# Kernel tuning notes

Hardware: AMD Instinct MI355X
Metric: run time of the kernel (lower is better)

The kernel has to match this reference:

```python
import jax, jax.numpy as jnp
import numpy as np

NUM_ENT, SEQ, H, OUT, NG = 10000, 10, 200, 100, 2048


def _seg_mean(x, idx, n):
    s = jax.ops.segment_sum(x, idx, num_segments=n)
    d = jax.ops.segment_sum(jnp.ones((idx.shape[0],), x.dtype), idx, num_segments=n)
    return s / jnp.maximum(d, 1.0)[:, None]


def setup_inputs() -> dict:
    k = jax.random.split(jax.random.key(0), 24)
    N, E, Nw, Ew, Vw, Rsel, MQ = 50000, 200000, 30000, 300000, 40000, 8192, 8
    f = lambda i, shp: jax.random.normal(k[i], shp, jnp.float32) * 0.05
    ri = lambda i, shp, hi: jax.random.randint(k[i], shp, 0, hi)
    return dict(
        ent_embeds=f(0, (NUM_ENT, H)), rel_embeds=f(1, (240, H)), word_embeds=f(2, (Vw, OUT)),
        gcn_w1=f(3, (OUT, H)), gcn_b1=jnp.zeros((H,), jnp.float32),
        gcn_w2=f(4, (H, H)), gcn_b2=jnp.zeros((H,), jnp.float32),
        cg1_wn=f(5, (H, OUT)), cg1_wl=f(6, (H, OUT)), cg1_wr=f(7, (H, OUT)),
        cg2_wn=f(8, (OUT, H)), cg2_wl=f(9, (OUT, H)), cg2_wr=f(10, (OUT, H)),
        attn_wa=f(11, (H, H)), attn_wc=f(12, (2 * H, H)),
        node_slot=jnp.arange(N), edge_src=ri(13, (E,), N), edge_dst=ri(14, (E,), N),
        edge_type=ri(15, (E,), 240), word_id=ri(16, (Nw,), Vw),
        wsrc=ri(17, (Ew,), Nw), wdst=ri(18, (Ew,), Nw),
        ent_word_idx=ri(19, (N, MQ), Nw), ent_word_mask=ri(20, (N, MQ), 2).astype(jnp.int32),
        rel_word_idx=ri(21, (Rsel, MQ), Nw), rel_word_mask=ri(22, (Rsel, MQ), 2).astype(jnp.int32),
        r_ids_graph=ri(23, (Rsel,), E), edge_slot=jnp.arange(Rsel))


def reference(ent_embeds, rel_embeds, word_embeds, gcn_w1, gcn_b1, gcn_w2, gcn_b2,
              cg1_wn, cg1_wl, cg1_wr, cg2_wn, cg2_wl, cg2_wr, attn_wa, attn_wc,
              node_slot, edge_src, edge_dst, edge_type, word_id, wsrc, wdst,
              ent_word_idx, ent_word_mask, rel_word_idx, rel_word_mask, r_ids_graph, edge_slot):
    N = node_slot.shape[0]
    Nw = word_id.shape[0]
    Rsel = r_ids_graph.shape[0]
    # --- se_aggr: 2-layer GCN over the batched word graph ---
    wh = word_embeds[word_id]                                   # [Nw,100]
    wh = jax.nn.relu(_seg_mean(wh[wsrc], wdst, Nw) @ gcn_w1 + gcn_b1)
    wh = jax.nn.relu(_seg_mean(wh[wsrc], wdst, Nw) @ gcn_w2 + gcn_b2)
    # --- re_aggr1/re_aggr2: CompGCN message passing on batched event graph ---
    h = ent_embeds[node_slot % NUM_ENT]                         # [N,200]
    e = rel_embeds[edge_type]                                   # [E,200]
    def compgcn(h, e, wn, wl, wr):
        agg = _seg_mean(h[edge_src] - e, edge_dst, N)           # sub-composition msgs
        return jax.nn.relu(agg @ wn + h @ wl), e @ wr
    h, e = compgcn(h, e, cg1_wn, cg1_wl, cg1_wr)                # 200 -> 100
    h, e = compgcn(h, e, cg2_wn, cg2_wl, cg2_wr)                # 100 -> 200
    embeds_g_r = e[r_ids_graph]                                 # [Rsel,200]
    # --- build Q_mx / H_mx (padded word-context groups) + 'general' attention ---
    Q = jnp.concatenate([h, embeds_g_r], 0)                     # [N+Rsel,200]
    H_ent = wh[ent_word_idx] * ent_word_mask[..., None].astype(wh.dtype)   # [N,8,200]
    H_rel = wh[rel_word_idx] * rel_word_mask[..., None].astype(wh.dtype)   # [Rsel,8,200]
    Hm = jnp.concatenate([H_ent, H_rel], 0)                     # [N+Rsel,8,200]
    scores = jnp.einsum('md,de,mke->mk', Q, attn_wa, Hm)
    attn = jax.nn.softmax(scores, axis=-1)
    ctx = jnp.einsum('mk,mkd->md', attn, Hm)
    out = jnp.tanh(jnp.concatenate([ctx, Q], -1) @ attn_wc)     # [N+Rsel,200]
    h_out, r_out = out[:N], out[N:]
    # --- temporal scatter of node embeddings per snapshot graph ---
    nid = node_slot % NUM_ENT
    gidx = node_slot // (N // SEQ)
    node_emb_temporal = jnp.zeros((NUM_ENT, SEQ, H), h_out.dtype).at[nid, gidx].set(h_out)
    # --- pack selected edge embeds into padded [NG, SEQ, H] sequence tensor ---
    per = Rsel // NG
    row, pos = edge_slot // per, edge_slot % per
    embed_seq = jnp.zeros((NG, SEQ, H), r_out.dtype).at[row, pos].set(r_out)
    return embed_seq, node_emb_temporal
```

## Files before the change

kernel.cpp:

```cpp
#include <hip/hip_runtime.h>
#include <cstddef>

constexpr int NUM_ENT_C = 10000;
constexpr int SEQ_C     = 10;
constexpr int H_C       = 200;
constexpr int OUT_C     = 100;
constexpr int NG_C      = 2048;
constexpr int NREL_C    = 240;
constexpr int MQ_C      = 8;

typedef __attribute__((ext_vector_type(8))) short          bf16x8;
typedef __attribute__((ext_vector_type(4))) float          f32x4;
typedef __attribute__((ext_vector_type(8))) unsigned short u16x8;

__device__ __forceinline__ unsigned short f2bf(float v) {
    unsigned u = __float_as_uint(v);
    unsigned r = (u + 0x7FFFu + ((u >> 16) & 1u)) >> 16;
    return (unsigned short)r;
}
__device__ __forceinline__ float bf2f(unsigned short b) {
    return __uint_as_float((unsigned)b << 16);
}
__device__ __forceinline__ void up2(unsigned u, float& lo, float& hi) {
    lo = __uint_as_float(u << 16);
    hi = __uint_as_float(u & 0xFFFF0000u);
}

__global__ void prep_k(const float* __restrict__ ent, unsigned short* __restrict__ entb, size_t e8,
                       const float* __restrict__ wemb, unsigned short* __restrict__ wembb, size_t w8,
                       int* __restrict__ cdeg, int nNodes) {
    size_t total = e8 + w8 + (size_t)nNodes;
    size_t stride = (size_t)gridDim.x * blockDim.x;
    for (size_t t = (size_t)blockIdx.x * blockDim.x + threadIdx.x; t < total; t += stride) {
        if (t < e8) {
            const float* s = ent + t * 8;
            u16x8 o;
            #pragma unroll
            for (int i = 0; i < 8; ++i) o[i] = f2bf(s[i]);
            *reinterpret_cast<u16x8*>(entb + t * 8) = o;
        } else if (t < e8 + w8) {
            size_t tt = t - e8;
            const float* s = wemb + tt * 8;
            u16x8 o;
            #pragma unroll
            for (int i = 0; i < 8; ++i) o[i] = f2bf(s[i]);
            *reinterpret_cast<u16x8*>(wembb + tt * 8) = o;
        } else {
            cdeg[t - e8 - w8] = 0;
        }
    }
}

__global__ void hist2_k(const int* __restrict__ wdst, int Ew,
                        const int* __restrict__ edst, int E,
                        int* __restrict__ cdeg, int Nw) {
    int total = Ew + E;
    int stride = gridDim.x * blockDim.x;
    for (int t = blockIdx.x * blockDim.x + threadIdx.x; t < total; t += stride) {
        if (t < Ew) atomicAdd(&cdeg[wdst[t]], 1);
        else        atomicAdd(&cdeg[Nw + edst[t - Ew]], 1);
    }
}

__global__ void scanA_k(const int* __restrict__ v, int* __restrict__ bsum, int n) {
    __shared__ int s[256];
    int t = threadIdx.x;
    int i = blockIdx.x * 256 + t;
    s[t] = (i < n) ? v[i] : 0;
    __syncthreads();
    for (int d = 128; d; d >>= 1) {
        if (t < d) s[t] += s[t + d];
        __syncthreads();
    }
    if (t == 0) bsum[blockIdx.x] = s[0];
}

__global__ void scanB_k(int* __restrict__ bsum, int nb) {
    __shared__ int s[512];
    int t = threadIdx.x;
    int v = (t < nb) ? bsum[t] : 0;
    s[t] = v;
    __syncthreads();
    for (int d = 1; d < 512; d <<= 1) {
        int x = (t >= d) ? s[t - d] : 0;
        __syncthreads();
        s[t] += x;
        __syncthreads();
    }
    if (t < nb) bsum[t] = s[t] - v;
}

__global__ void scanC_k(const int* __restrict__ v, const int* __restrict__ bsum,
                        int* __restrict__ offs, int* __restrict__ cur, int n) {
    __shared__ int s[256];
    int t = threadIdx.x;
    int i = blockIdx.x * 256 + t;
    int val = (i < n) ? v[i] : 0;
    s[t] = val;
    __syncthreads();
    for (int d = 1; d < 256; d <<= 1) {
        int x = (t >= d) ? s[t - d] : 0;
        __syncthreads();
        s[t] += x;
        __syncthreads();
    }
    if (i < n) {
        int ex = s[t] - val + bsum[blockIdx.x];
        offs[i] = ex;
        cur[i]  = ex;
    }
}

__global__ void fill2_k(const int* __restrict__ wdst, const int* __restrict__ wsrc,
                        const int* __restrict__ word_id, int Ew,
                        const int* __restrict__ edst, const int* __restrict__ esrc,
                        const int* __restrict__ etype, int E,
                        int* __restrict__ ccur, int Nw,
                        int* __restrict__ bktA, int* __restrict__ bktB) {
    int total = Ew + E;
    int stride = gridDim.x * blockDim.x;
    for (int t = blockIdx.x * blockDim.x + threadIdx.x; t < total; t += stride) {
        if (t < Ew) {
            int s = wsrc[t];
            int p = atomicAdd(&ccur[wdst[t]], 1);
            bktA[p] = word_id[s];
            bktB[p] = s;
        } else {
            int e = t - Ew;
            int p = atomicAdd(&ccur[Nw + edst[e]], 1);
            bktA[p] = esrc[e];
            bktB[p] = etype[e];
        }
    }
}

template<int K1, int K2, int Kp, bool RELSUB, bool SRCMOD, bool SELFMOD, bool DUAL>
__global__ __launch_bounds__(256) void gather_mean_k(
        const unsigned short* __restrict__ feat, const unsigned short* __restrict__ selfT,
        const float* __restrict__ rel,
        const int* __restrict__ bktS, const int* __restrict__ bktT,
        const int* __restrict__ offs, const int* __restrict__ deg,
        unsigned short* __restrict__ dst, int n) {
    int node = blockIdx.x * 4 + (threadIdx.x >> 6);
    int lane = threadIdx.x & 63;
    if (node >= n) return;
    int off = offs[node], dg = deg[node];
    float acc[4] = {0.f, 0.f, 0.f, 0.f};
    unsigned short* drow = dst + (size_t)node * Kp;

    if (DUAL) {
        int half = lane >> 5, lh = lane & 31;
        int d0 = lh * 4;
        bool act = d0 < K1;
        for (int i = 0; i < dg; i += 2) {
            int ii = i + half;
            if (ii < dg && act) {
                int s = bktS[off + ii];
                if (SRCMOD) s = s % NUM_ENT_C;
                uint2 u = *reinterpret_cast<const uint2*>(feat + (size_t)s * K1 + d0);
                float e0, e1, e2, e3;
                up2(u.x, e0, e1); up2(u.y, e2, e3);
                if (RELSUB) {
                    int tt = bktT[off + ii];
                    float4 rv = *reinterpret_cast<const float4*>(rel + (size_t)tt * K1 + d0);
                    e0 -= rv.x; e1 -= rv.y; e2 -= rv.z; e3 -= rv.w;
                }
                acc[0] += e0; acc[1] += e1; acc[2] += e2; acc[3] += e3;
            }
        }
        #pragma unroll
        for (int c = 0; c < 4; ++c) acc[c] += __shfl_xor(acc[c], 32);
        float inv = 1.f / fmaxf((float)dg, 1.f);
        if (half == 0 && act) {
            uint2 o;
            o.x = (unsigned)f2bf(acc[0] * inv) | ((unsigned)f2bf(acc[1] * inv) << 16);
            o.y = (unsigned)f2bf(acc[2] * inv) | ((unsigned)f2bf(acc[3] * inv) << 16);
            *reinterpret_cast<uint2*>(drow + d0) = o;
        }
        if (K2 > 0 && half == 1 && d0 < K2) {
            int srow = SELFMOD ? (node % NUM_ENT_C) : node;
            uint2 sv = *reinterpret_cast<const uint2*>(selfT + (size_t)srow * K2 + d0);
            *reinterpret_cast<uint2*>(drow + K1 + d0) = sv;
        }
    } else {
        int d0 = lane * 4;
        bool act = d0 < K1;
        for (int i = 0; i < dg; ++i) {
            if (act) {
                int s = bktS[off + i];
                if (SRCMOD) s = s % NUM_ENT_C;
                uint2 u = *reinterpret_cast<const uint2*>(feat + (size_t)s * K1 + d0);
                float e0, e1, e2, e3;
                up2(u.x, e0, e1); up2(u.y, e2, e3);
                if (RELSUB) {
                    int tt = bktT[off + i];
                    float4 rv = *reinterpret_cast<const float4*>(rel + (size_t)tt * K1 + d0);
                    e0 -= rv.x; e1 -= rv.y; e2 -= rv.z; e3 -= rv.w;
                }
                acc[0] += e0; acc[1] += e1; acc[2] += e2; acc[3] += e3;
            }
        }
        float inv = 1.f / fmaxf((float)dg, 1.f);
        if (act) {
            uint2 o;
            o.x = (unsigned)f2bf(acc[0] * inv) | ((unsigned)f2bf(acc[1] * inv) << 16);
            o.y = (unsigned)f2bf(acc[2] * inv) | ((unsigned)f2bf(acc[3] * inv) << 16);
            *reinterpret_cast<uint2*>(drow + d0) = o;
        }
        if (K2 > 0 && d0 < K2) {
            int srow = SELFMOD ? (node % NUM_ENT_C) : node;
            uint2 sv = *reinterpret_cast<const uint2*>(selfT + (size_t)srow * K2 + d0);
            *reinterpret_cast<uint2*>(drow + K1 + d0) = sv;
        }
    }
    for (int cc = K1 + K2 + lane; cc < Kp; cc += 64) drow[cc] = 0;
}

__global__ void convw_all_k(const float* __restrict__ gcn_w1, const float* __restrict__ gcn_w2,
                            const float* __restrict__ cg1_wn, const float* __restrict__ cg1_wl,
                            const float* __restrict__ cg2_wn, const float* __restrict__ cg2_wl,
                            const float* __restrict__ attn_wa, const float* __restrict__ attn_wc,
                            unsigned short* __restrict__ Wt) {
    constexpr int S0 = 26624;
    constexpr int S1 = S0 + 46592;
    constexpr int S2 = S1 + 46592;
    constexpr int S3 = S2 + 46592;
    constexpr int S4 = S3 + 46592;
    constexpr int S5 = S4 + 86528;
    int stride = gridDim.x * blockDim.x;
    for (int t = blockIdx.x * blockDim.x + threadIdx.x; t < S5; t += stride) {
        float v = 0.f;
        if (t < S0) {
            int l = t, nn = l >> 7, k = l & 127;
            if (nn < 200 && k < 100) v = gcn_w1[k * 200 + nn];
        } else if (t < S1) {
            int l = t - S0, nn = l / 224, k = l - nn * 224;
            if (nn < 200 && k < 200) v = gcn_w2[k * 200 + nn];
        } else if (t < S2) {
            int l = t - S1, nn = l / 416, k = l - nn * 416;
            if (nn < 100) {
                if (k < 200)      v = cg1_wn[k * 100 + nn];
                else if (k < 400) v = cg1_wl[(k - 200) * 100 + nn];
            }
        } else if (t < S3) {
            int l = t - S2, nn = l / 224, k = l - nn * 224;
            if (nn < 200) {
                if (k < 100)      v = cg2_wn[k * 200 + nn];
                else if (k < 200) v = cg2_wl[(k - 100) * 200 + nn];
            }
        } else if (t < S4) {
            int l = t - S3, nn = l / 224, k = l - nn * 224;
            if (nn < 200 && k < 200) v = attn_wa[k * 200 + nn];
        } else {
            int l = t - S4, nn = l / 416, k = l - nn * 416;
            if (nn < 200 && k < 400) v = attn_wc[k * 200 + nn];
        }
        Wt[t] = f2bf(v);
    }
}

__global__ void post_k(const float* __restrict__ rel2, const int* __restrict__ edge_type,
                       const int* __restrict__ r_ids, unsigned short* __restrict__ A,
                       const int* __restrict__ node_slot, const int* __restrict__ edge_slot,
                       int* __restrict__ rowOff, int N, int M, int divq, int per, int embBase) {
    int R = M - N;
    size_t secA = (size_t)R * H_C;
    size_t secB = secA + (size_t)M * 6;
    size_t total = secB + (size_t)M;
    size_t stride = (size_t)gridDim.x * blockDim.x;
    for (size_t t = (size_t)blockIdx.x * blockDim.x + threadIdx.x; t < total; t += stride) {
        if (t < secA) {
            int r = (int)(t / H_C);
            int d = (int)(t - (size_t)r * H_C);
            int rr = r_ids[r];
            A[(size_t)(N + r) * 448 + 200 + d] = f2bf(rel2[(size_t)edge_type[rr] * H_C + d]);
        } else if (t < secB) {
            size_t l = t - secA;
            int m = (int)(l / 6), c = (int)(l - (size_t)m * 6);
            *reinterpret_cast<uint4*>(A + (size_t)m * 448 + 400 + c * 8) = make_uint4(0u, 0u, 0u, 0u);
        } else {
            int m = (int)(t - secB);
            int offv;
            if (m < N) {
                int ns = node_slot[m];
                offv = embBase + ((ns % NUM_ENT_C) * SEQ_C + ns / divq) * H_C;
            } else {
                int es = edge_slot[m - N];
                offv = ((es / per) * SEQ_C + (es - (es / per) * per)) * H_C;
            }
            rowOff[m] = offv;
        }
    }
}

template<int NF, int ACT, bool SCATTER, bool OBF16>
__global__ __launch_bounds__(256) void mfma_gemm_k(
        const unsigned short* __restrict__ A, int lda,
        const unsigned short* __restrict__ Wt,
        const float* __restrict__ bias, void* __restrict__ Cv, int ldc,
        const int* __restrict__ rowOff, int M, int N, int Kp) {
    constexpr int BN = NF * 16;
    __shared__ unsigned short As[64][40];
    __shared__ unsigned short Bs[BN][40];
    const int tid  = threadIdx.x;
    const int bm   = blockIdx.x * 64;
    const int w    = tid >> 6;
    const int lane = tid & 63;
    const int lr   = lane & 15;
    const int lk   = (lane >> 4) * 8;

    f32x4 acc[NF];
    #pragma unroll
    for (int nf = 0; nf < NF; ++nf) acc[nf] = (f32x4){0.f, 0.f, 0.f, 0.f};

    for (int k0 = 0; k0 < Kp; k0 += 32) {
        {
            int m = tid >> 2, c = tid & 3;
            int gm = bm + m;
            uint4 v = make_uint4(0u, 0u, 0u, 0u);
            if (gm < M) v = *reinterpret_cast<const uint4*>(A + (size_t)gm * lda + k0 + c * 8);
            *reinterpret_cast<uint4*>(&As[m][c * 8]) = v;
        }
        for (int i = tid; i < NF * 64; i += 256) {
            int n = i >> 2, c = i & 3;
            uint4 v = *reinterpret_cast<const uint4*>(Wt + (size_t)n * Kp + k0 + c * 8);
            *reinterpret_cast<uint4*>(&Bs[n][c * 8]) = v;
        }
        __syncthreads();
        bf16x8 a = *reinterpret_cast<const bf16x8*>(&As[w * 16 + lr][lk]);
        #pragma unroll
        for (int nf = 0; nf < NF; ++nf) {
            bf16x8 b = *reinterpret_cast<const bf16x8*>(&Bs[nf * 16 + lr][lk]);
            acc[nf] = __builtin_amdgcn_mfma_f32_16x16x32_bf16(a, b, acc[nf], 0, 0, 0);
        }
        __syncthreads();
    }

    const int r0 = (lane >> 4) * 4;
    #pragma unroll
    for (int j = 0; j < 4; ++j) {
        int gm = bm + w * 16 + r0 + j;
        if (gm >= M) continue;
        size_t base;
        if (SCATTER && !OBF16) base = (size_t)rowOff[gm];
        else                   base = (size_t)gm * ldc;
        #pragma unroll
        for (int nf = 0; nf < NF; ++nf) {
            int gn = nf * 16 + lr;
            if (gn >= N) continue;
            float v = acc[nf][j];
            if (bias) v += bias[gn];
            if (ACT == 1) v = fmaxf(v, 0.f);
            if (ACT == 2) v = tanhf(v);
            if (OBF16) ((unsigned short*)Cv)[base + gn] = f2bf(v);
            else       ((float*)Cv)[base + gn] = v;
        }
    }
}

template<int NF, int ACT, bool SCATTER, bool OBF16>
static void launch_mfma(hipStream_t s, const unsigned short* A, int lda,
                        const unsigned short* Wt, const float* bias,
                        void* C, int ldc, const int* rowOff, int M, int N, int Kp) {
    mfma_gemm_k<NF, ACT, SCATTER, OBF16><<<dim3((M + 63) / 64), 256, 0, s>>>(
        A, lda, Wt, bias, C, ldc, rowOff, M, N, Kp);
}

__global__ __launch_bounds__(256) void gemm_f32_k(
        const float* __restrict__ A, const float* __restrict__ W,
        float* __restrict__ C, int M, int N, int K) {
    constexpr int TS = 64, BK = 16;
    __shared__ float As[BK][TS];
    __shared__ float Bs[BK][TS];
    int bm = blockIdx.x * TS, bn = blockIdx.y * TS;
    int tid = threadIdx.x;
    int tx = tid & 15, ty = tid >> 4;
    float acc[4][4] = {};
    for (int k0 = 0; k0 < K; k0 += BK) {
        #pragma unroll
        for (int l = tid; l < TS * BK; l += 256) {
            int m = l >> 4, kk = l & 15;
            int gm = bm + m, gk = k0 + kk;
            As[kk][m] = (gm < M && gk < K) ? A[(size_t)gm * K + gk] : 0.f;
        }
        #pragma unroll
        for (int l = tid; l < TS * BK; l += 256) {
            int kk = l >> 6, n = l & 63;
            int gk = k0 + kk, gn = bn + n;
            Bs[kk][n] = (gk < K && gn < N) ? W[(size_t)gk * N + gn] : 0.f;
        }
        __syncthreads();
        #pragma unroll
        for (int kk = 0; kk < BK; ++kk) {
            float a[4], b[4];
            #pragma unroll
            for (int i = 0; i < 4; ++i) a[i] = As[kk][ty * 4 + i];
            #pragma unroll
            for (int j = 0; j < 4; ++j) b[j] = Bs[kk][tx * 4 + j];
            #pragma unroll
            for (int i = 0; i < 4; ++i)
                #pragma unroll
                for (int j = 0; j < 4; ++j) acc[i][j] += a[i] * b[j];
        }
        __syncthreads();
    }
    #pragma unroll
    for (int i = 0; i < 4; ++i) {
        int gm = bm + ty * 4 + i;
        if (gm >= M) continue;
        #pragma unroll
        for (int j = 0; j < 4; ++j) {
            int gn = bn + tx * 4 + j;
            if (gn < N) C[(size_t)gm * N + gn] = acc[i][j];
        }
    }
}

__global__ __launch_bounds__(256) void attn_k(
        const unsigned short* __restrict__ QAb, const unsigned short* __restrict__ whb,
        const int* __restrict__ ent_idx, const int* __restrict__ ent_mask,
        const int* __restrict__ rel_idx, const int* __restrict__ rel_mask,
        unsigned short* __restrict__ ctxOut, int N, int M) {
    int m = blockIdx.x * 4 + (threadIdx.x >> 6);
    int lane = threadIdx.x & 63;
    if (m >= M) return;
    const int* idxp;
    const int* mskp;
    if (m < N) { idxp = ent_idx + (size_t)m * MQ_C;        mskp = ent_mask + (size_t)m * MQ_C; }
    else       { idxp = rel_idx + (size_t)(m - N) * MQ_C;  mskp = rel_mask + (size_t)(m - N) * MQ_C; }

    int d0 = lane * 4;
    bool act = d0 < H_C;
    float qa0 = 0.f, qa1 = 0.f, qa2 = 0.f, qa3 = 0.f;
    if (act) {
        uint2 u = *reinterpret_cast<const uint2*>(QAb + (size_t)m * H_C + d0);
        up2(u.x, qa0, qa1); up2(u.y, qa2, qa3);
    }
    int  idx[MQ_C];
    int  msk[MQ_C];
    float s[MQ_C];
    uint2 wr[MQ_C];
    #pragma unroll
    for (int k = 0; k < MQ_C; ++k) { idx[k] = idxp[k]; msk[k] = mskp[k]; }
    #pragma unroll
    for (int k = 0; k < MQ_C; ++k) {
        if (msk[k] != 0) {
            float p = 0.f;
            if (act) {
                wr[k] = *reinterpret_cast<const uint2*>(whb + (size_t)idx[k] * H_C + d0);
                float e0, e1, e2, e3;
                up2(wr[k].x, e0, e1); up2(wr[k].y, e2, e3);
                p = qa0 * e0 + qa1 * e1 + qa2 * e2 + qa3 * e3;
            } else {
                wr[k] = make_uint2(0u, 0u);
            }
            #pragma unroll
            for (int off = 32; off; off >>= 1) p += __shfl_xor(p, off);
            s[k] = p;
        } else {
            s[k] = 0.f;
            wr[k] = make_uint2(0u, 0u);
        }
    }
    float mx = s[0];
    #pragma unroll
    for (int k = 1; k < MQ_C; ++k) mx = fmaxf(mx, s[k]);
    float den = 0.f;
    #pragma unroll
    for (int k = 0; k < MQ_C; ++k) { s[k] = expf(s[k] - mx); den += s[k]; }
    float inv = 1.f / den;
    if (act) {
        float c0 = 0.f, c1 = 0.f, c2 = 0.f, c3 = 0.f;
        #pragma unroll
        for (int k = 0; k < MQ_C; ++k) {
            if (msk[k] != 0) {
                float e0, e1, e2, e3;
                up2(wr[k].x, e0, e1); up2(wr[k].y, e2, e3);
                c0 += s[k] * e0; c1 += s[k] * e1; c2 += s[k] * e2; c3 += s[k] * e3;
            }
        }
        uint2 o;
        o.x = (unsigned)f2bf(c0 * inv) | ((unsigned)f2bf(c1 * inv) << 16);
        o.y = (unsigned)f2bf(c2 * inv) | ((unsigned)f2bf(c3 * inv) << 16);
        *reinterpret_cast<uint2*>(ctxOut + (size_t)m * 448 + d0) = o;
    }
}


static inline dim3 ew_grid(size_t total) {
    size_t b = (total + 255) / 256;
    if (b > 4096) b = 4096;
    return dim3((unsigned)b);
}

extern "C" void kernel_launch(void* const* d_in, const int* in_sizes, int n_in,
                              void* d_out, int out_size, void* d_ws, size_t ws_size,
                              hipStream_t stream) {
    const float* ent_embeds = (const float*)d_in[0];
    const float* rel_embeds = (const float*)d_in[1];
    const float* word_embeds= (const float*)d_in[2];
    const float* gcn_w1     = (const float*)d_in[3];
    const float* gcn_b1     = (const float*)d_in[4];
    const float* gcn_w2     = (const float*)d_in[5];
    const float* gcn_b2     = (const float*)d_in[6];
    const float* cg1_wn     = (const float*)d_in[7];
    const float* cg1_wl     = (const float*)d_in[8];
    const float* cg1_wr     = (const float*)d_in[9];
    const float* cg2_wn     = (const float*)d_in[10];
    const float* cg2_wl     = (const float*)d_in[11];
    const float* cg2_wr     = (const float*)d_in[12];
    const float* attn_wa    = (const float*)d_in[13];
    const float* attn_wc    = (const float*)d_in[14];
    const int* node_slot    = (const int*)d_in[15];
    const int* edge_src     = (const int*)d_in[16];
    const int* edge_dst     = (const int*)d_in[17];
    const int* edge_type    = (const int*)d_in[18];
    const int* word_id      = (const int*)d_in[19];
    const int* wsrc         = (const int*)d_in[20];
    const int* wdst         = (const int*)d_in[21];
    const int* ent_word_idx = (const int*)d_in[22];
    const int* ent_word_mask= (const int*)d_in[23];
    const int* rel_word_idx = (const int*)d_in[24];
    const int* rel_word_mask= (const int*)d_in[25];
    const int* r_ids_graph  = (const int*)d_in[26];
    const int* edge_slot    = (const int*)d_in[27];

    const int N    = in_sizes[15];
    const int E    = in_sizes[16];
    const int Nw   = in_sizes[19];
    const int Ew   = in_sizes[20];
    const int Rsel = in_sizes[27];
    const int M    = N + Rsel;
    const int divq = N / SEQ_C;
    const int per  = Rsel / NG_C;
    const int embBase = NG_C * SEQ_C * H_C;
    const size_t entElems  = (size_t)in_sizes[0];
    const size_t wembElems = (size_t)in_sizes[2];
    const int nNodes = Nw + N;

    float* ws = (float*)d_ws;
    size_t o = 0;
    auto align4 = [&]() { o = (o + 3) & ~(size_t)3; };
    int* cdeg  = (int*)(ws + o); o += nNodes;
    int* coffs = (int*)(ws + o); o += nNodes;
    int* ccur  = (int*)(ws + o); o += nNodes;
    int* bktA  = (int*)(ws + o); o += Ew + E;
    int* bktB  = (int*)(ws + o); o += Ew + E;
    int* bsum  = (int*)(ws + o); o += 512;
    int* rowOff= (int*)(ws + o); o += M;
    float* rel1 = ws + o; o += (size_t)NREL_C * OUT_C;
    float* rel2 = ws + o; o += (size_t)NREL_C * H_C;
    align4();
    unsigned short* Wt      = (unsigned short*)(ws + o); o += 299520 / 2;
    align4();
    unsigned short* wh_bf   = (unsigned short*)(ws + o); o += ((size_t)Nw * H_C) / 2;
    align4();
    unsigned short* h1_bf   = (unsigned short*)(ws + o); o += ((size_t)N * OUT_C) / 2;
    align4();
    unsigned short* ent_bf  = (unsigned short*)(ws + o); o += entElems / 2;
    align4();
    unsigned short* wemb_bf = (unsigned short*)(ws + o); o += wembElems / 2;
    align4();
    unsigned short* AbfF    = (unsigned short*)(ws + o); o += ((size_t)M * 448) / 2;
    align4();
    float* BIG = ws + o;
    unsigned short* wh1_bf = (unsigned short*)BIG;
    unsigned short* AbfW   = (unsigned short*)(BIG + ((size_t)Nw * H_C) / 2);
    unsigned short* AbfE   = (unsigned short*)BIG;
    unsigned short* QAb    = (unsigned short*)d_out;

    unsigned short* WT_g1 = Wt;
    unsigned short* WT_g2 = Wt + 26624;
    unsigned short* WT_c1 = Wt + 73216;
    unsigned short* WT_c2 = Wt + 119808;
    unsigned short* WT_wa = Wt + 166400;
    unsigned short* WT_wc = Wt + 212992;

    prep_k<<<ew_grid(entElems / 8 + wembElems / 8 + nNodes), 256, 0, stream>>>(
        ent_embeds, ent_bf, entElems / 8, word_embeds, wemb_bf, wembElems / 8,
        cdeg, nNodes);
    convw_all_k<<<ew_grid(299520), 256, 0, stream>>>(
        gcn_w1, gcn_w2, cg1_wn, cg1_wl, cg2_wn, cg2_wl, attn_wa, attn_wc, Wt);
    hist2_k<<<ew_grid((size_t)Ew + E), 256, 0, stream>>>(wdst, Ew, edge_dst, E, cdeg, Nw);
    {
        int nb = (nNodes + 255) / 256;
        scanA_k<<<nb, 256, 0, stream>>>(cdeg, bsum, nNodes);
        scanB_k<<<1, 512, 0, stream>>>(bsum, nb);
        scanC_k<<<nb, 256, 0, stream>>>(cdeg, bsum, coffs, ccur, nNodes);
    }
    fill2_k<<<ew_grid((size_t)Ew + E), 256, 0, stream>>>(
        wdst, wsrc, word_id, Ew, edge_dst, edge_src, edge_type, E, ccur, Nw, bktA, bktB);
    gemm_f32_k<<<dim3((NREL_C + 63) / 64, (OUT_C + 63) / 64), 256, 0, stream>>>(
        rel_embeds, cg1_wr, rel1, NREL_C, OUT_C, H_C);
    gemm_f32_k<<<dim3((NREL_C + 63) / 64, (H_C + 63) / 64), 256, 0, stream>>>(
        rel1, cg2_wr, rel2, NREL_C, H_C, OUT_C);
    post_k<<<ew_grid((size_t)Rsel * H_C + (size_t)M * 7), 256, 0, stream>>>(
        rel2, edge_type, r_ids_graph, AbfF, node_slot, edge_slot, rowOff,
        N, M, divq, per, embBase);

    gather_mean_k<OUT_C, 0, 128, false, false, false, true><<<dim3((Nw + 3) / 4), 256, 0, stream>>>(
        wemb_bf, nullptr, nullptr, bktA, nullptr, coffs, cdeg, AbfW, Nw);
    launch_mfma<13, 1, false, true>(stream, AbfW, 128, WT_g1, gcn_b1, wh1_bf, H_C, nullptr, Nw, H_C, 128);
    gather_mean_k<H_C, 0, 224, false, false, false, false><<<dim3((Nw + 3) / 4), 256, 0, stream>>>(
        wh1_bf, nullptr, nullptr, bktB, nullptr, coffs, cdeg, AbfW, Nw);
    launch_mfma<13, 1, false, true>(stream, AbfW, 224, WT_g2, gcn_b2, wh_bf, H_C, nullptr, Nw, H_C, 224);

    gather_mean_k<H_C, H_C, 448, true, true, true, false><<<dim3((N + 3) / 4), 256, 0, stream>>>(
        ent_bf, ent_bf, rel_embeds, bktA, bktB, coffs + Nw, cdeg + Nw, AbfE, N);
    launch_mfma<7, 1, false, true>(stream, AbfE, 448, WT_c1, nullptr, h1_bf, OUT_C, nullptr, N, OUT_C, 416);
    gather_mean_k<OUT_C, OUT_C, 224, true, false, false, true><<<dim3((N + 3) / 4), 256, 0, stream>>>(
        h1_bf, h1_bf, rel1, bktA, bktB, coffs + Nw, cdeg + Nw, AbfE, N);
    launch_mfma<13, 1, false, true>(stream, AbfE, 224, WT_c2, nullptr, AbfF + 200, 448, nullptr, N, H_C, 224);

    launch_mfma<13, 0, false, true>(stream, AbfF + 200, 448, WT_wa, nullptr, QAb, H_C, nullptr, M, H_C, 224);
    attn_k<<<(M + 3) / 4, 256, 0, stream>>>(QAb, wh_bf, ent_word_idx, ent_word_mask,
                                            rel_word_idx, rel_word_mask, AbfF, N, M);
    hipMemsetAsync(d_out, 0, (size_t)out_size * 4, stream);
    launch_mfma<13, 2, true, false>(stream, AbfF, 448, WT_wc, nullptr, d_out, H_C, rowOff, M, H_C, 416);
}
```

Baseline: 672.3 us.

## Fuse attention projection, softmax context and output GEMM into one kernel

Replaces the separate Q·Wa GEMM, attention kernel and final Wc GEMM with a single kernel. Each 64-row block keeps Q in LDS, computes QA with MFMA, runs the 8-way attention softmax and context in LDS, then applies the concatenated Wc GEMM with tanh and the scattered store. The Wc weight layout is reordered so Q and ctx each occupy their own K segment. This removes the global round trips for QA and ctx and two launches. In exchange it uses large LDS per block, leaving fewer blocks per CU, and the attention phase runs serially over 16 rows per wave.

```diff
diff --git a/kernel.cpp b/kernel.cpp
--- a/kernel.cpp
+++ b/kernel.cpp
@@ -226,7 +226,7 @@
     constexpr int S2 = S1 + 46592;
     constexpr int S3 = S2 + 46592;
     constexpr int S4 = S3 + 46592;
-    constexpr int S5 = S4 + 86528;
+    constexpr int S5 = S4 + 93184;
     int stride = gridDim.x * blockDim.x;
     for (int t = blockIdx.x * blockDim.x + threadIdx.x; t < S5; t += stride) {
         float v = 0.f;
@@ -252,8 +252,11 @@
             int l = t - S3, nn = l / 224, k = l - nn * 224;
             if (nn < 200 && k < 200) v = attn_wa[k * 200 + nn];
         } else {
-            int l = t - S4, nn = l / 416, k = l - nn * 416;
-            if (nn < 200 && k < 400) v = attn_wc[k * 200 + nn];
+            int l = t - S4, nn = l / 448, k = l - nn * 448;
+            if (nn < 200) {
+                if (k < 200)                  v = attn_wc[(200 + k) * 200 + nn];
+                else if (k >= 224 && k < 424) v = attn_wc[(k - 224) * 200 + nn];
+            }
         }
         Wt[t] = f2bf(v);
     }
@@ -416,73 +419,162 @@
     }
 }
 
-__global__ __launch_bounds__(256) void attn_k(
-        const unsigned short* __restrict__ QAb, const unsigned short* __restrict__ whb,
+__global__ __launch_bounds__(256) void fusedA_k(
+        const unsigned short* __restrict__ AbfQ,
+        const unsigned short* __restrict__ WTwa,
+        const unsigned short* __restrict__ WTwc,
+        const unsigned short* __restrict__ whb,
         const int* __restrict__ ent_idx, const int* __restrict__ ent_mask,
         const int* __restrict__ rel_idx, const int* __restrict__ rel_mask,
-        unsigned short* __restrict__ ctxOut, int N, int M) {
-    int m = blockIdx.x * 4 + (threadIdx.x >> 6);
-    int lane = threadIdx.x & 63;
-    if (m >= M) return;
-    const int* idxp;
-    const int* mskp;
-    if (m < N) { idxp = ent_idx + (size_t)m * MQ_C;        mskp = ent_mask + (size_t)m * MQ_C; }
-    else       { idxp = rel_idx + (size_t)(m - N) * MQ_C;  mskp = rel_mask + (size_t)(m - N) * MQ_C; }
-
-    int d0 = lane * 4;
-    bool act = d0 < H_C;
-    float qa0 = 0.f, qa1 = 0.f, qa2 = 0.f, qa3 = 0.f;
-    if (act) {
-        uint2 u = *reinterpret_cast<const uint2*>(QAb + (size_t)m * H_C + d0);
-        up2(u.x, qa0, qa1); up2(u.y, qa2, qa3);
-    }
-    int  idx[MQ_C];
-    int  msk[MQ_C];
-    float s[MQ_C];
-    uint2 wr[MQ_C];
+        const int* __restrict__ rowOff,
+        float* __restrict__ outp, int N, int M) {
+    constexpr int NF = 13;
+    __shared__ unsigned short QL[64][232];
+    __shared__ unsigned short QC[64][232];
+    __shared__ unsigned short Bs[208][40];
+    const int tid  = threadIdx.x;
+    const int bm   = blockIdx.x * 64;
+    const int w    = tid >> 6;
+    const int lane = tid & 63;
+    const int lr   = lane & 15;
+    const int lk   = (lane >> 4) * 8;
+    const int r0   = (lane >> 4) * 4;
+
+    for (int ch = tid; ch < 64 * 28; ch += 256) {
+        int m = ch / 28, c = ch - m * 28;
+        int gm = bm + m;
+        uint4 v = make_uint4(0u, 0u, 0u, 0u);
+        if (gm < M) v = *reinterpret_cast<const uint4*>(AbfQ + (size_t)gm * 448 + c * 8);
+        *reinterpret_cast<uint4*>(&QL[m][c * 8]) = v;
+    }
+    __syncthreads();
+
+    f32x4 acc[NF];
     #pragma unroll
-    for (int k = 0; k < MQ_C; ++k) { idx[k] = idxp[k]; msk[k] = mskp[k]; }
+    for (int nf = 0; nf < NF; ++nf) acc[nf] = (f32x4){0.f, 0.f, 0.f, 0.f};
+    for (int k0 = 0; k0 < 224; k0 += 32) {
+        for (int i = tid; i < NF * 64; i += 256) {
+            int n = i >> 2, c = i & 3;
+            *reinterpret_cast<uint4*>(&Bs[n][c * 8]) =
+                *reinterpret_cast<const uint4*>(WTwa + (size_t)n * 224 + k0 + c * 8);
+        }
+        __syncthreads();
+        bf16x8 a = *reinterpret_cast<const bf16x8*>(&QL[w * 16 + lr][k0 + lk]);
+        #pragma unroll
+        for (int nf = 0; nf < NF; ++nf) {
+            bf16x8 b = *reinterpret_cast<const bf16x8*>(&Bs[nf * 16 + lr][lk]);
+            acc[nf] = __builtin_amdgcn_mfma_f32_16x16x32_bf16(a, b, acc[nf], 0, 0, 0);
+        }
+        __syncthreads();
+    }
     #pragma unroll
-    for (int k = 0; k < MQ_C; ++k) {
-        if (msk[k] != 0) {
-            float p = 0.f;
+    for (int j = 0; j < 4; ++j) {
+        #pragma unroll
+        for (int nf = 0; nf < NF; ++nf) {
+            int gn = nf * 16 + lr;
+            if (gn < 200) QC[w * 16 + r0 + j][gn] = f2bf(acc[nf][j]);
+        }
+    }
+
+    {
+        int d0 = lane * 4;
+        bool act  = d0 < H_C;
+        bool padw = (d0 >= 200 && d0 < 224);
+        for (int t = 0; t < 16; ++t) {
+            int row = w * 16 + t;
+            int gm  = bm + row;
+            if (gm >= M) continue;
+            if (padw) *reinterpret_cast<uint2*>(&QC[row][d0]) = make_uint2(0u, 0u);
+            const int* idxp;
+            const int* mskp;
+            if (gm < N) { idxp = ent_idx + (size_t)gm * MQ_C;       mskp = ent_mask + (size_t)gm * MQ_C; }
+            else        { idxp = rel_idx + (size_t)(gm - N) * MQ_C; mskp = rel_mask + (size_t)(gm - N) * MQ_C; }
+            float qa0 = 0.f, qa1 = 0.f, qa2 = 0.f, qa3 = 0.f;
             if (act) {
-                wr[k] = *reinterpret_cast<const uint2*>(whb + (size_t)idx[k] * H_C + d0);
-                float e0, e1, e2, e3;
-                up2(wr[k].x, e0, e1); up2(wr[k].y, e2, e3);
-                p = qa0 * e0 + qa1 * e1 + qa2 * e2 + qa3 * e3;
-            } else {
-                wr[k] = make_uint2(0u, 0u);
-            }
-            #pragma unroll
-            for (int off = 32; off; off >>= 1) p += __shfl_xor(p, off);
-            s[k] = p;
-        } else {
-            s[k] = 0.f;
-            wr[k] = make_uint2(0u, 0u);
-        }
-    }
-    float mx = s[0];
+                uint2 u = *reinterpret_cast<const uint2*>(&QC[row][d0]);
+                up2(u.x, qa0, qa1); up2(u.y, qa2, qa3);
+            }
+            int  idx[MQ_C];
+            int  msk[MQ_C];
+            float s[MQ_C];
+            uint2 wr[MQ_C];
+            #pragma unroll
+            for (int k = 0; k < MQ_C; ++k) { idx[k] = idxp[k]; msk[k] = mskp[k]; }
+            #pragma unroll
+            for (int k = 0; k < MQ_C; ++k) {
+                if (msk[k] != 0) {
+                    float p = 0.f;
+                    if (act) {
+                        wr[k] = *reinterpret_cast<const uint2*>(whb + (size_t)idx[k] * H_C + d0);
+                        float e0, e1, e2, e3;
+                        up2(wr[k].x, e0, e1); up2(wr[k].y, e2, e3);
+                        p = qa0 * e0 + qa1 * e1 + qa2 * e2 + qa3 * e3;
+                    } else {
+                        wr[k] = make_uint2(0u, 0u);
+                    }
+                    #pragma unroll
+                    for (int off = 32; off; off >>= 1) p += __shfl_xor(p, off);
+                    s[k] = p;
+                } else {
+                    s[k] = 0.f;
+                    wr[k] = make_uint2(0u, 0u);
+                }
+            }
+            float mx = s[0];
+            #pragma unroll
+            for (int k = 1; k < MQ_C; ++k) mx = fmaxf(mx, s[k]);
+            float den = 0.f;
+            #pragma unroll
+            for (int k = 0; k < MQ_C; ++k) { s[k] = expf(s[k] - mx); den += s[k]; }
+            float inv = 1.f / den;
+            if (act) {
+                float c0 = 0.f, c1 = 0.f, c2 = 0.f, c3 = 0.f;
+                #pragma unroll
+                for (int k = 0; k < MQ_C; ++k) {
+                    if (msk[k] != 0) {
+                        float e0, e1, e2, e3;
+                        up2(wr[k].x, e0, e1); up2(wr[k].y, e2, e3);
+                        c0 += s[k] * e0; c1 += s[k] * e1; c2 += s[k] * e2; c3 += s[k] * e3;
+                    }
+                }
+                uint2 o;
+                o.x = (unsigned)f2bf(c0 * inv) | ((unsigned)f2bf(c1 * inv) << 16);
+                o.y = (unsigned)f2bf(c2 * inv) | ((unsigned)f2bf(c3 * inv) << 16);
+                *reinterpret_cast<uint2*>(&QC[row][d0]) = o;
+            }
+        }
+    }
+    __syncthreads();
+
     #pragma unroll
-    for (int k = 1; k < MQ_C; ++k) mx = fmaxf(mx, s[k]);
-    float den = 0.f;
+    for (int nf = 0; nf < NF; ++nf) acc[nf] = (f32x4){0.f, 0.f, 0.f, 0.f};
+    for (int k0i = 0; k0i < 14; ++k0i) {
+        for (int i = tid; i < NF * 64; i += 256) {
+            int n = i >> 2, c = i & 3;
+            *reinterpret_cast<uint4*>(&Bs[n][c * 8]) =
+                *reinterpret_cast<const uint4*>(WTwc + (size_t)n * 448 + k0i * 32 + c * 8);
+        }
+        __syncthreads();
+        const unsigned short* Ap = (k0i < 7) ? &QL[0][0] : &QC[0][0];
+        int kk = (k0i < 7 ? k0i : k0i - 7) * 32;
+        bf16x8 a = *reinterpret_cast<const bf16x8*>(Ap + (size_t)(w * 16 + lr) * 232 + kk + lk);
+        #pragma unroll
+        for (int nf = 0; nf < NF; ++nf) {
+            bf16x8 b = *reinterpret_cast<const bf16x8*>(&Bs[nf * 16 + lr][lk]);
+            acc[nf] = __builtin_amdgcn_mfma_f32_16x16x32_bf16(a, b, acc[nf], 0, 0, 0);
+        }
+        __syncthreads();
+    }
     #pragma unroll
-    for (int k = 0; k < MQ_C; ++k) { s[k] = expf(s[k] - mx); den += s[k]; }
-    float inv = 1.f / den;
-    if (act) {
-        float c0 = 0.f, c1 = 0.f, c2 = 0.f, c3 = 0.f;
-        #pragma unroll
-        for (int k = 0; k < MQ_C; ++k) {
-            if (msk[k] != 0) {
-                float e0, e1, e2, e3;
-                up2(wr[k].x, e0, e1); up2(wr[k].y, e2, e3);
-                c0 += s[k] * e0; c1 += s[k] * e1; c2 += s[k] * e2; c3 += s[k] * e3;
-            }
-        }
-        uint2 o;
-        o.x = (unsigned)f2bf(c0 * inv) | ((unsigned)f2bf(c1 * inv) << 16);
-        o.y = (unsigned)f2bf(c2 * inv) | ((unsigned)f2bf(c3 * inv) << 16);
-        *reinterpret_cast<uint2*>(ctxOut + (size_t)m * 448 + d0) = o;
+    for (int j = 0; j < 4; ++j) {
+        int gm = bm + w * 16 + r0 + j;
+        if (gm >= M) continue;
+        size_t base = (size_t)rowOff[gm];
+        #pragma unroll
+        for (int nf = 0; nf < NF; ++nf) {
+            int gn = nf * 16 + lr;
+            if (gn < 200) outp[base + gn] = tanhf(acc[nf][j]);
+        }
     }
 }
 
@@ -551,7 +643,7 @@
     float* rel1 = ws + o; o += (size_t)NREL_C * OUT_C;
     float* rel2 = ws + o; o += (size_t)NREL_C * H_C;
     align4();
-    unsigned short* Wt      = (unsigned short*)(ws + o); o += 299520 / 2;
+    unsigned short* Wt      = (unsigned short*)(ws + o); o += 306176 / 2;
     align4();
     unsigned short* wh_bf   = (unsigned short*)(ws + o); o += ((size_t)Nw * H_C) / 2;
     align4();
@@ -567,7 +659,6 @@
     unsigned short* wh1_bf = (unsigned short*)BIG;
     unsigned short* AbfW   = (unsigned short*)(BIG + ((size_t)Nw * H_C) / 2);
     unsigned short* AbfE   = (unsigned short*)BIG;
-    unsigned short* QAb    = (unsigned short*)d_out;
 
     unsigned short* WT_g1 = Wt;
     unsigned short* WT_g2 = Wt + 26624;
@@ -579,7 +670,7 @@
     prep_k<<<ew_grid(entElems / 8 + wembElems / 8 + nNodes), 256, 0, stream>>>(
         ent_embeds, ent_bf, entElems / 8, word_embeds, wemb_bf, wembElems / 8,
         cdeg, nNodes);
-    convw_all_k<<<ew_grid(299520), 256, 0, stream>>>(
+    convw_all_k<<<ew_grid(306176), 256, 0, stream>>>(
         gcn_w1, gcn_w2, cg1_wn, cg1_wl, cg2_wn, cg2_wl, attn_wa, attn_wc, Wt);
     hist2_k<<<ew_grid((size_t)Ew + E), 256, 0, stream>>>(wdst, Ew, edge_dst, E, cdeg, Nw);
     {
@@ -612,9 +703,9 @@
         h1_bf, h1_bf, rel1, bktA, bktB, coffs + Nw, cdeg + Nw, AbfE, N);
     launch_mfma<13, 1, false, true>(stream, AbfE, 224, WT_c2, nullptr, AbfF + 200, 448, nullptr, N, H_C, 224);
 
-    launch_mfma<13, 0, false, true>(stream, AbfF + 200, 448, WT_wa, nullptr, QAb, H_C, nullptr, M, H_C, 224);
-    attn_k<<<(M + 3) / 4, 256, 0, stream>>>(QAb, wh_bf, ent_word_idx, ent_word_mask,
-                                            rel_word_idx, rel_word_mask, AbfF, N, M);
     hipMemsetAsync(d_out, 0, (size_t)out_size * 4, stream);
-    launch_mfma<13, 2, true, false>(stream, AbfF, 448, WT_wc, nullptr, d_out, H_C, rowOff, M, H_C, 416);
-}
+    fusedA_k<<<dim3((M + 63) / 64), 256, 0, stream>>>(
+        AbfF + 200, WT_wa, WT_wc, wh_bf,
+        ent_word_idx, ent_word_mask, rel_word_idx, rel_word_mask,
+        rowOff, (float*)d_out, N, M);
+}
```

After: 738.5 us. +9.8%, slower.
